# Kernel optimization log

Hardware: AMD Instinct MI355X
Metric: run time of the kernel (lower is better)

Reference implementation:

```python
import jax, jax.numpy as jnp
import numpy as np

T = 2_000_000  # seq_len
I, H, O = 2, 30, 1  # input_size, hidden_size, output_size


def setup_inputs() -> dict:
    key = jax.random.key(0)
    ks = jax.random.split(key, 7)
    s = 1.0 / np.sqrt(H)  # torch default uniform(-1/sqrt(H), 1/sqrt(H)) scale
    return {
        "x": jax.random.normal(ks[0], (T, I), dtype=jnp.float32),
        "W_ih": jax.random.uniform(ks[1], (H, I), jnp.float32, -s, s),
        "W_hh": jax.random.uniform(ks[2], (H, H), jnp.float32, -s, s),
        "b_ih": jax.random.uniform(ks[3], (H,), jnp.float32, -s, s),
        "b_hh": jax.random.uniform(ks[4], (H,), jnp.float32, -s, s),
        "W_fc": jax.random.uniform(ks[5], (O, H), jnp.float32, -s, s),
        "b_fc": jax.random.uniform(ks[6], (O,), jnp.float32, -s, s),
    }


def reference(x, W_ih, W_hh, b_ih, b_hh, W_fc, b_fc):
    # Elman RNN (torch.nn.RNN, tanh): h_t = tanh(x_t W_ih^T + b_ih + h_{t-1} W_hh^T + b_hh)
    # Precompute the input projection for all timesteps in one GEMM.
    xp = x @ W_ih.T + (b_ih + b_hh)  # [T, H]

    def step(h, xt):
        h = jnp.tanh(xt + h @ W_hh.T)
        return h, h

    h0 = jnp.zeros((H,), dtype=x.dtype)
    _, hs = jax.lax.scan(step, h0, xp)  # hs: [T, H]
    return hs @ W_fc.T + b_fc  # [T, O]
```

## Files before the change

kernel.cpp:

```cpp
#include <hip/hip_runtime.h>


#define T_LEN     2000000
#define HID       30
#define CHUNK_LEN 64
#define BURN      23
#define BPW       16
#define NBLOCK    512
#define WSTEPS    8
#define NWIN      11

typedef __attribute__((ext_vector_type(4))) _Float16 half4;
typedef __attribute__((ext_vector_type(4))) float    float4v;

#define STAGE_LOAD(o) {                                                      \
    int t0 = st_base_t + (o) * WSTEPS + st_j;                                \
    int t1 = t0 + 4;                                                         \
    t0 = t0 < 0 ? 0 : (t0 >= T_LEN ? T_LEN - 1 : t0);                        \
    t1 = t1 < 0 ? 0 : (t1 >= T_LEN ? T_LEN - 1 : t1);                        \
    stv0 = ((const float2*)x)[t0];                                           \
    stv1 = ((const float2*)x)[t1];                                           \
}
#define STAGE_WRITE(o) {                                                     \
    union { unsigned u; _Float16 h[2]; } c0, c1;                             \
    c0.h[0] = (_Float16)stv0.x; c0.h[1] = (_Float16)stv0.y;                  \
    c1.h[0] = (_Float16)stv1.x; c1.h[1] = (_Float16)stv1.y;                  \
    const int wb = ((o) & 1) * 512;                                          \
    lds_x[wb + st_j * 64 + st_chunk_local]       = c0.u;                     \
    lds_x[wb + (st_j + 4) * 64 + st_chunk_local] = c1.u;                     \
}

#define STEP(s, MASKQ, STOREQ)                                               \
{                                                                            \
    unsigned xn = 0u;                                                        \
    if ((s) < WSTEPS - 1) xn = lds_x[rb + ((s) + 1) * 64];                   \
    float th_t[4], th_b[4];                                                  \
    _Pragma("unroll")                                                        \
    for (int i = 0; i < 4; ++i) {                                            \
        th_t[i] = 1.f - 2.f * __builtin_amdgcn_rcpf(1.f + __builtin_amdgcn_exp2f(d_t[i])); \
        th_b[i] = 1.f - 2.f * __builtin_amdgcn_rcpf(1.f + __builtin_amdgcn_exp2f(d_b[i])); \
    }                                                                        \
    if (MASKQ) {                                                             \
        const float m = (t_cur >= 1) ? 1.f : 0.f;                            \
        _Pragma("unroll")                                                    \
        for (int i = 0; i < 4; ++i) { th_t[i] *= m; th_b[i] *= m; }          \
    }                                                                        \
    half4 b0, b1;                                                            \
    _Pragma("unroll")                                                        \
    for (int i = 0; i < 4; ++i) { b0[i] = (_Float16)th_t[i]; b1[i] = (_Float16)th_b[i]; } \
    if (g3) {                                                                \
        union { unsigned u; _Float16 h[2]; } cv; cv.u = xc;                  \
        b1[2] = cv.h[0]; b1[3] = cv.h[1];                                    \
    }                                                                        \
    d_t = __builtin_amdgcn_mfma_f32_16x16x16f16(a_t0, b0, cT, 0, 0, 0);      \
    d_b = __builtin_amdgcn_mfma_f32_16x16x16f16(a_b0, b0, cB, 0, 0, 0);      \
    d_t = __builtin_amdgcn_mfma_f32_16x16x16f16(a_t1, b1, d_t, 0, 0, 0);     \
    d_b = __builtin_amdgcn_mfma_f32_16x16x16f16(a_b1, b1, d_b, 0, 0, 0);     \
    if (STOREQ) {                                                            \
        if (g3 && (t_cur - 1) < my_end) out[t_cur - 1] = d_b[2];             \
    }                                                                        \
    xc = xn;                                                                 \
    ++t_cur;                                                                 \
}

#define WINDOW(o, MASKQ, STOREQ, LASTQ)                                      \
{                                                                            \
    const int rb = ((o) & 1) * 512 + chunk_local;                            \
    unsigned xc = lds_x[rb];                                                 \
    if (!(LASTQ)) STAGE_LOAD((o) + 1)                                        \
    STEP(0, MASKQ, STOREQ) STEP(1, MASKQ, STOREQ)                            \
    STEP(2, MASKQ, STOREQ) STEP(3, MASKQ, STOREQ)                            \
    STEP(4, MASKQ, STOREQ) STEP(5, MASKQ, STOREQ)                            \
    STEP(6, MASKQ, STOREQ) STEP(7, MASKQ, STOREQ)                            \
    if (!(LASTQ)) STAGE_WRITE((o) + 1)                                       \
    __syncthreads();                                                         \
}

__global__ __launch_bounds__(256, 2)
void rnn_mfma_kernel(const float* __restrict__ x,
                     const float* __restrict__ W_ih,
                     const float* __restrict__ W_hh,
                     const float* __restrict__ b_ih,
                     const float* __restrict__ b_hh,
                     const float* __restrict__ W_fc,
                     const float* __restrict__ b_fc,
                     float* __restrict__ out)
{
    __shared__ unsigned lds_x[2 * WSTEPS * 64];

    const int tid  = threadIdx.x;
    const int wave = tid >> 6;
    const int lane = tid & 63;
    const int g    = lane >> 4;
    const int cl   = lane & 15;
    const bool g3  = (g == 3);
    const int chunk_local = wave * BPW + cl;
    const int chunk = blockIdx.x * 64 + chunk_local;

    const int st_chunk_local = tid >> 2;
    const int st_j           = tid & 3;
    const int st_base_t = (blockIdx.x * 64 + st_chunk_local) * CHUNK_LEN - BURN;

    const float SC = 2.0f * 1.44269504088896340736f;

    half4 a_t0, a_t1, a_b0, a_b1;
#pragma unroll
    for (int i = 0; i < 4; ++i) {
        const int k0 = 4*g + i;
        const int k1 = 16 + 4*g + i;
        const int mt = cl;
        const int mb = 16 + cl;

        a_t0[i] = (_Float16)(SC * W_hh[mt*HID + k0]);
        float v_t1;
        if (k1 < HID)        v_t1 = SC * W_hh[mt*HID + k1];
        else if (k1 == HID)  v_t1 = SC * W_ih[mt*2 + 0];
        else                 v_t1 = SC * W_ih[mt*2 + 1];
        a_t1[i] = (_Float16)v_t1;

        float v_b0, v_b1;
        if (mb < HID) {
            v_b0 = SC * W_hh[mb*HID + k0];
            if (k1 < HID)        v_b1 = SC * W_hh[mb*HID + k1];
            else if (k1 == HID)  v_b1 = SC * W_ih[mb*2 + 0];
            else                 v_b1 = SC * W_ih[mb*2 + 1];
        } else if (mb == HID) {
            v_b0 = W_fc[k0];
            v_b1 = (k1 < HID) ? W_fc[k1] : 0.f;
        } else {
            v_b0 = 0.f; v_b1 = 0.f;
        }
        a_b0[i] = (_Float16)v_b0;
        a_b1[i] = (_Float16)v_b1;
    }

    float4v cT, cB;
#pragma unroll
    for (int i = 0; i < 4; ++i) {
        const int rt = 4*g + i;
        const int rb2 = 16 + 4*g + i;
        cT[i] = SC * (b_ih[rt] + b_hh[rt]);
        cB[i] = (rb2 < HID)  ? SC * (b_ih[rb2] + b_hh[rb2])
              : (rb2 == HID) ? b_fc[0] : 0.f;
    }

    const int t_ws = chunk * CHUNK_LEN;
    int my_end = t_ws + CHUNK_LEN; if (my_end > T_LEN) my_end = T_LEN;

    __builtin_amdgcn_sched_barrier(0);

    float4v d_t = {0.f, 0.f, 0.f, 0.f};
    float4v d_b = {0.f, 0.f, 0.f, 0.f};

    int t_cur = t_ws - BURN;

    float2 stv0, stv1;
    STAGE_LOAD(0)
    STAGE_WRITE(0)
    __syncthreads();

    WINDOW(0, true, false, false)
    WINDOW(1, true, false, false)
    WINDOW(2, true, false, false)
    WINDOW(3, false, true, false)
    WINDOW(4, false, true, false)
    WINDOW(5, false, true, false)
    WINDOW(6, false, true, false)
    WINDOW(7, false, true, false)
    WINDOW(8, false, true, false)
    WINDOW(9, false, true, false)
    WINDOW(10, false, true, true)
}

extern "C" void kernel_launch(void* const* d_in, const int* in_sizes, int n_in,
                              void* d_out, int out_size, void* d_ws, size_t ws_size,
                              hipStream_t stream)
{
    const float* x    = (const float*)d_in[0];
    const float* W_ih = (const float*)d_in[1];
    const float* W_hh = (const float*)d_in[2];
    const float* b_ih = (const float*)d_in[3];
    const float* b_hh = (const float*)d_in[4];
    const float* W_fc = (const float*)d_in[5];
    const float* b_fc = (const float*)d_in[6];
    float* out = (float*)d_out;

    rnn_mfma_kernel<<<NBLOCK, 256, 0, stream>>>(x, W_ih, W_hh, b_ih, b_hh,
                                                W_fc, b_fc, out);
}
```

Measured before the change: 100.6 us.

## Interleave two independent RNN chunks per wave and halve the chunk length

Each lane group now advances two independent 32-step chunks (A and B) in lockstep. Their MFMA and tanh sequences are interleaved to hide dependency latency, and the serial step count per thread drops from 88 to 56. The x staging buffer and the loader are widened to 128 chunks per block. Float-to-half conversions now use packed round-toward-zero converts. The trade-off is a larger burn-in overhead relative to useful steps, and slightly different rounding from the RTZ conversion.

```diff
diff --git a/kernel.cpp b/kernel.cpp
--- a/kernel.cpp
+++ b/kernel.cpp
@@ -3,75 +3,101 @@
 
 #define T_LEN     2000000
 #define HID       30
-#define CHUNK_LEN 64
+#define CHUNK_LEN 32
 #define BURN      23
-#define BPW       16
 #define NBLOCK    512
 #define WSTEPS    8
-#define NWIN      11
 
 typedef __attribute__((ext_vector_type(4))) _Float16 half4;
+typedef __attribute__((ext_vector_type(2))) __fp16   fp16x2;
 typedef __attribute__((ext_vector_type(4))) float    float4v;
 
+union h4u { half4 v4; fp16x2 v2[2]; unsigned u2[2]; };
+union h2u { fp16x2 v; unsigned u; };
+
 #define STAGE_LOAD(o) {                                                      \
-    int t0 = st_base_t + (o) * WSTEPS + st_j;                                \
-    int t1 = t0 + 4;                                                         \
-    t0 = t0 < 0 ? 0 : (t0 >= T_LEN ? T_LEN - 1 : t0);                        \
-    t1 = t1 < 0 ? 0 : (t1 >= T_LEN ? T_LEN - 1 : t1);                        \
-    stv0 = ((const float2*)x)[t0];                                           \
-    stv1 = ((const float2*)x)[t1];                                           \
+    const int tb = st_base_t + (o) * WSTEPS;                                 \
+    int i0 = tb + st_j,     i1 = tb + st_j + 1;                              \
+    int i2 = tb + st_j + 4, i3 = tb + st_j + 5;                              \
+    i0 = i0 < 0 ? 0 : (i0 >= T_LEN ? T_LEN - 1 : i0);                        \
+    i1 = i1 < 0 ? 0 : (i1 >= T_LEN ? T_LEN - 1 : i1);                        \
+    i2 = i2 < 0 ? 0 : (i2 >= T_LEN ? T_LEN - 1 : i2);                        \
+    i3 = i3 < 0 ? 0 : (i3 >= T_LEN ? T_LEN - 1 : i3);                        \
+    stv0 = ((const float2*)x)[i0]; stv1 = ((const float2*)x)[i1];            \
+    stv2 = ((const float2*)x)[i2]; stv3 = ((const float2*)x)[i3];            \
 }
 #define STAGE_WRITE(o) {                                                     \
-    union { unsigned u; _Float16 h[2]; } c0, c1;                             \
-    c0.h[0] = (_Float16)stv0.x; c0.h[1] = (_Float16)stv0.y;                  \
-    c1.h[0] = (_Float16)stv1.x; c1.h[1] = (_Float16)stv1.y;                  \
-    const int wb = ((o) & 1) * 512;                                          \
-    lds_x[wb + st_j * 64 + st_chunk_local]       = c0.u;                     \
-    lds_x[wb + (st_j + 4) * 64 + st_chunk_local] = c1.u;                     \
-}
-
-#define STEP(s, MASKQ, STOREQ)                                               \
+    const int wb = ((o) & 1) * 1024;                                         \
+    h2u c0, c1, c2, c3;                                                      \
+    c0.v = __builtin_amdgcn_cvt_pkrtz(stv0.x, stv0.y);                       \
+    c1.v = __builtin_amdgcn_cvt_pkrtz(stv1.x, stv1.y);                       \
+    c2.v = __builtin_amdgcn_cvt_pkrtz(stv2.x, stv2.y);                       \
+    c3.v = __builtin_amdgcn_cvt_pkrtz(stv3.x, stv3.y);                       \
+    lds_x[wb + (st_j + 0) * 128 + st_c] = c0.u;                              \
+    lds_x[wb + (st_j + 1) * 128 + st_c] = c1.u;                              \
+    lds_x[wb + (st_j + 4) * 128 + st_c] = c2.u;                              \
+    lds_x[wb + (st_j + 5) * 128 + st_c] = c3.u;                              \
+}
+
+#define STEP2(s, MASKQ, STOREQ)                                              \
 {                                                                            \
-    unsigned xn = 0u;                                                        \
-    if ((s) < WSTEPS - 1) xn = lds_x[rb + ((s) + 1) * 64];                   \
-    float th_t[4], th_b[4];                                                  \
+    unsigned xnA = 0u, xnB = 0u;                                             \
+    if ((s) < WSTEPS - 1) {                                                  \
+        xnA = lds_x[rbA + ((s) + 1) * 128];                                  \
+        xnB = lds_x[rbB + ((s) + 1) * 128];                                  \
+    }                                                                        \
+    float tA[8], tB[8];                                                      \
     _Pragma("unroll")                                                        \
     for (int i = 0; i < 4; ++i) {                                            \
-        th_t[i] = 1.f - 2.f * __builtin_amdgcn_rcpf(1.f + __builtin_amdgcn_exp2f(d_t[i])); \
-        th_b[i] = 1.f - 2.f * __builtin_amdgcn_rcpf(1.f + __builtin_amdgcn_exp2f(d_b[i])); \
+        tA[i]   = 1.f - 2.f * __builtin_amdgcn_rcpf(1.f + __builtin_amdgcn_exp2f(d_tA[i])); \
+        tA[4+i] = 1.f - 2.f * __builtin_amdgcn_rcpf(1.f + __builtin_amdgcn_exp2f(d_bA[i])); \
+        tB[i]   = 1.f - 2.f * __builtin_amdgcn_rcpf(1.f + __builtin_amdgcn_exp2f(d_tB[i])); \
+        tB[4+i] = 1.f - 2.f * __builtin_amdgcn_rcpf(1.f + __builtin_amdgcn_exp2f(d_bB[i])); \
     }                                                                        \
     if (MASKQ) {                                                             \
+        \
         const float m = (t_cur >= 1) ? 1.f : 0.f;                            \
         _Pragma("unroll")                                                    \
-        for (int i = 0; i < 4; ++i) { th_t[i] *= m; th_b[i] *= m; }          \
-    }                                                                        \
-    half4 b0, b1;                                                            \
-    _Pragma("unroll")                                                        \
-    for (int i = 0; i < 4; ++i) { b0[i] = (_Float16)th_t[i]; b1[i] = (_Float16)th_b[i]; } \
-    if (g3) {                                                                \
-        union { unsigned u; _Float16 h[2]; } cv; cv.u = xc;                  \
-        b1[2] = cv.h[0]; b1[3] = cv.h[1];                                    \
-    }                                                                        \
-    d_t = __builtin_amdgcn_mfma_f32_16x16x16f16(a_t0, b0, cT, 0, 0, 0);      \
-    d_b = __builtin_amdgcn_mfma_f32_16x16x16f16(a_b0, b0, cB, 0, 0, 0);      \
-    d_t = __builtin_amdgcn_mfma_f32_16x16x16f16(a_t1, b1, d_t, 0, 0, 0);     \
-    d_b = __builtin_amdgcn_mfma_f32_16x16x16f16(a_b1, b1, d_b, 0, 0, 0);     \
+        for (int i = 0; i < 8; ++i) tA[i] *= m;                              \
+    }                                                                        \
+    h4u b0A, b1A, b0B, b1B;                                                  \
+    b0A.v2[0] = __builtin_amdgcn_cvt_pkrtz(tA[0], tA[1]);                    \
+    b0A.v2[1] = __builtin_amdgcn_cvt_pkrtz(tA[2], tA[3]);                    \
+    b1A.v2[0] = __builtin_amdgcn_cvt_pkrtz(tA[4], tA[5]);                    \
+    b1A.v2[1] = __builtin_amdgcn_cvt_pkrtz(tA[6], tA[7]);                    \
+    b0B.v2[0] = __builtin_amdgcn_cvt_pkrtz(tB[0], tB[1]);                    \
+    b0B.v2[1] = __builtin_amdgcn_cvt_pkrtz(tB[2], tB[3]);                    \
+    b1B.v2[0] = __builtin_amdgcn_cvt_pkrtz(tB[4], tB[5]);                    \
+    b1B.v2[1] = __builtin_amdgcn_cvt_pkrtz(tB[6], tB[7]);                    \
+    if (g3) { b1A.u2[1] = xcA; b1B.u2[1] = xcB; }                            \
+    d_tA = __builtin_amdgcn_mfma_f32_16x16x16f16(a_t0, b0A.v4, cT, 0, 0, 0); \
+    d_bA = __builtin_amdgcn_mfma_f32_16x16x16f16(a_b0, b0A.v4, cB, 0, 0, 0); \
+    d_tB = __builtin_amdgcn_mfma_f32_16x16x16f16(a_t0, b0B.v4, cT, 0, 0, 0); \
+    d_bB = __builtin_amdgcn_mfma_f32_16x16x16f16(a_b0, b0B.v4, cB, 0, 0, 0); \
+    d_tA = __builtin_amdgcn_mfma_f32_16x16x16f16(a_t1, b1A.v4, d_tA, 0, 0, 0); \
+    d_bA = __builtin_amdgcn_mfma_f32_16x16x16f16(a_b1, b1A.v4, d_bA, 0, 0, 0); \
+    d_tB = __builtin_amdgcn_mfma_f32_16x16x16f16(a_t1, b1B.v4, d_tB, 0, 0, 0); \
+    d_bB = __builtin_amdgcn_mfma_f32_16x16x16f16(a_b1, b1B.v4, d_bB, 0, 0, 0); \
     if (STOREQ) {                                                            \
-        if (g3 && (t_cur - 1) < my_end) out[t_cur - 1] = d_b[2];             \
-    }                                                                        \
-    xc = xn;                                                                 \
+        const int ta = t_cur - 1;                                            \
+        if (g3 && ta < my_endA) out[ta] = d_bA[2];                           \
+        const int tb2 = ta + 16 * CHUNK_LEN;                                 \
+        if (g3 && tb2 < my_endB) out[tb2] = d_bB[2];                         \
+    }                                                                        \
+    xcA = xnA; xcB = xnB;                                                    \
     ++t_cur;                                                                 \
 }
 
 #define WINDOW(o, MASKQ, STOREQ, LASTQ)                                      \
 {                                                                            \
-    const int rb = ((o) & 1) * 512 + chunk_local;                            \
-    unsigned xc = lds_x[rb];                                                 \
+    const int wb  = ((o) & 1) * 1024;                                        \
+    const int rbA = wb + rdA, rbB = wb + rdB;                                \
+    unsigned xcA = lds_x[rbA], xcB = lds_x[rbB];                             \
     if (!(LASTQ)) STAGE_LOAD((o) + 1)                                        \
-    STEP(0, MASKQ, STOREQ) STEP(1, MASKQ, STOREQ)                            \
-    STEP(2, MASKQ, STOREQ) STEP(3, MASKQ, STOREQ)                            \
-    STEP(4, MASKQ, STOREQ) STEP(5, MASKQ, STOREQ)                            \
-    STEP(6, MASKQ, STOREQ) STEP(7, MASKQ, STOREQ)                            \
+    STEP2(0, MASKQ, STOREQ) STEP2(1, MASKQ, STOREQ)                          \
+    STEP2(2, MASKQ, STOREQ) STEP2(3, MASKQ, STOREQ)                          \
+    STEP2(4, MASKQ, STOREQ) STEP2(5, MASKQ, STOREQ)                          \
+    STEP2(6, MASKQ, STOREQ) STEP2(7, MASKQ, STOREQ)                          \
     if (!(LASTQ)) STAGE_WRITE((o) + 1)                                       \
     __syncthreads();                                                         \
 }
@@ -86,7 +112,7 @@
                      const float* __restrict__ b_fc,
                      float* __restrict__ out)
 {
-    __shared__ unsigned lds_x[2 * WSTEPS * 64];
+    __shared__ unsigned lds_x[2 * WSTEPS * 128];
 
     const int tid  = threadIdx.x;
     const int wave = tid >> 6;
@@ -94,12 +120,15 @@
     const int g    = lane >> 4;
     const int cl   = lane & 15;
     const bool g3  = (g == 3);
-    const int chunk_local = wave * BPW + cl;
-    const int chunk = blockIdx.x * 64 + chunk_local;
-
-    const int st_chunk_local = tid >> 2;
-    const int st_j           = tid & 3;
-    const int st_base_t = (blockIdx.x * 64 + st_chunk_local) * CHUNK_LEN - BURN;
+
+    const int rdA = wave * 32 + cl;
+    const int rdB = rdA + 16;
+    const int chunkA = blockIdx.x * 128 + rdA;
+    const int chunkB = chunkA + 16;
+
+    const int st_c = tid >> 1;
+    const int st_j = (tid & 1) * 2;
+    const int st_base_t = (blockIdx.x * 128 + st_c) * CHUNK_LEN - BURN;
 
     const float SC = 2.0f * 1.44269504088896340736f;
 
@@ -137,39 +166,37 @@
     float4v cT, cB;
 #pragma unroll
     for (int i = 0; i < 4; ++i) {
-        const int rt = 4*g + i;
+        const int rt  = 4*g + i;
         const int rb2 = 16 + 4*g + i;
         cT[i] = SC * (b_ih[rt] + b_hh[rt]);
         cB[i] = (rb2 < HID)  ? SC * (b_ih[rb2] + b_hh[rb2])
               : (rb2 == HID) ? b_fc[0] : 0.f;
     }
 
-    const int t_ws = chunk * CHUNK_LEN;
-    int my_end = t_ws + CHUNK_LEN; if (my_end > T_LEN) my_end = T_LEN;
+    int my_endA = chunkA * CHUNK_LEN + CHUNK_LEN;
+    if (my_endA > T_LEN) my_endA = T_LEN;
+    int my_endB = chunkB * CHUNK_LEN + CHUNK_LEN;
+    if (my_endB > T_LEN) my_endB = T_LEN;
 
     __builtin_amdgcn_sched_barrier(0);
 
-    float4v d_t = {0.f, 0.f, 0.f, 0.f};
-    float4v d_b = {0.f, 0.f, 0.f, 0.f};
-
-    int t_cur = t_ws - BURN;
-
-    float2 stv0, stv1;
+    float4v d_tA = {0.f,0.f,0.f,0.f}, d_bA = {0.f,0.f,0.f,0.f};
+    float4v d_tB = {0.f,0.f,0.f,0.f}, d_bB = {0.f,0.f,0.f,0.f};
+
+    int t_cur = chunkA * CHUNK_LEN - BURN;
+
+    float2 stv0, stv1, stv2, stv3;
     STAGE_LOAD(0)
     STAGE_WRITE(0)
     __syncthreads();
 
-    WINDOW(0, true, false, false)
-    WINDOW(1, true, false, false)
-    WINDOW(2, true, false, false)
-    WINDOW(3, false, true, false)
-    WINDOW(4, false, true, false)
-    WINDOW(5, false, true, false)
-    WINDOW(6, false, true, false)
-    WINDOW(7, false, true, false)
-    WINDOW(8, false, true, false)
-    WINDOW(9, false, true, false)
-    WINDOW(10, false, true, true)
+    WINDOW(0, true,  false, false)
+    WINDOW(1, true,  false, false)
+    WINDOW(2, true,  false, false)
+    WINDOW(3, false, true,  false)
+    WINDOW(4, false, true,  false)
+    WINDOW(5, false, true,  false)
+    WINDOW(6, false, true,  true)
 }
 
 extern "C" void kernel_launch(void* const* d_in, const int* in_sizes, int n_in,
```

Result: slower. 105.7 us (+5.0%).
